# Optimization experiments

Measured on AMD Instinct MI355X. Metric: run time of the kernel, lower is better.

Reference implementation:

```python
import jax, jax.numpy as jnp
import numpy as np

D_MODEL = 512
HIDDEN = 2048
NUM_EXPERTS = 8
TOP_K = 2
BATCH, SEQ = 4, 4096


def setup_inputs() -> dict:
    key = jax.random.key(0)
    kx, kg, k1, k2 = jax.random.split(key, 4)
    x = jax.random.normal(kx, (BATCH, SEQ, D_MODEL), dtype=jnp.float32)
    # gate: nn.Linear(d_model, num_experts, bias=False), init std=0.02
    Wg = 0.02 * jax.random.normal(kg, (NUM_EXPERTS, D_MODEL), dtype=jnp.float32)
    # expert weights, xavier_uniform scale
    lim1 = float(np.sqrt(6.0 / (D_MODEL + HIDDEN)))
    lim2 = float(np.sqrt(6.0 / (HIDDEN + D_MODEL)))
    W1 = jax.random.uniform(k1, (NUM_EXPERTS, D_MODEL, HIDDEN), dtype=jnp.float32, minval=-lim1, maxval=lim1)
    W2 = jax.random.uniform(k2, (NUM_EXPERTS, HIDDEN, D_MODEL), dtype=jnp.float32, minval=-lim2, maxval=lim2)
    return {"x": x, "Wg": Wg, "W1": W1, "W2": W2}


def reference(x, Wg, W1, W2):
    B, S, d = x.shape
    E = W1.shape[0]
    xf = x.reshape(-1, d)  # [T, d]
    router_logits = xf @ Wg.T  # [T, E]
    # top-k routing, softmax over selected logits
    topv, sel = jax.lax.top_k(router_logits, TOP_K)  # [T, K]
    rw = jax.nn.softmax(topv, axis=-1)  # [T, K]
    # dense combine weights [T, E]: weight for expert e if selected, else 0
    cw = jnp.sum(jax.nn.one_hot(sel, E, dtype=xf.dtype) * rw[..., None], axis=1)
    # per-expert MLP (loop over small fixed E), weighted combine
    out = jnp.zeros_like(xf)
    for e in range(E):
        h = jax.nn.gelu(xf @ W1[e], approximate=False)  # exact erf GELU like nn.GELU
        out = out + cw[:, e:e + 1] * (h @ W2[e])
    return out.reshape(B, S, d), router_logits.reshape(B, S, E)
```

## Files before the change

kernel.cpp:

```cpp
#include <hip/hip_runtime.h>
#include <hip/hip_bf16.h>
#include <math.h>

#define T_TOK 16384
#define DM 512
#define HID 2048
#define NE 8
#define MT 64
#define CH 256
#define NCH (HID / CH)

typedef unsigned short u16;
typedef unsigned long long u64;
typedef __attribute__((ext_vector_type(4))) float f32x4;
typedef __attribute__((ext_vector_type(8))) __bf16 bf16x8;

static __device__ __forceinline__ u16 f2bf(float f) {
    __hip_bfloat16 h = __float2bfloat16(f);
    union { __hip_bfloat16 h; u16 u; } c; c.h = h; return c.u;
}

static __device__ __forceinline__ bf16x8 as_bf16x8(uint4 u) {
    union { uint4 u; bf16x8 b; } c; c.u = u; return c.b;
}

__global__ __launch_bounds__(256) void transpose_cvt(const float* __restrict__ in,
                                                     u16* __restrict__ out, int R, int C) {
    __shared__ float tile[64][65];
    const float* inp = in + (size_t)blockIdx.z * R * C;
    u16* outp = out + (size_t)blockIdx.z * R * C;
    int c0 = blockIdx.x * 64, r0 = blockIdx.y * 64;
    int tr = threadIdx.x >> 4;
    int tc = threadIdx.x & 15;
#pragma unroll
    for (int i = 0; i < 4; i++) {
        int r = i * 16 + tr;
        float4 v = *(const float4*)(inp + (size_t)(r0 + r) * C + c0 + tc * 4);
        tile[r][tc * 4 + 0] = v.x; tile[r][tc * 4 + 1] = v.y;
        tile[r][tc * 4 + 2] = v.z; tile[r][tc * 4 + 3] = v.w;
    }
    __syncthreads();
#pragma unroll
    for (int i = 0; i < 4; i++) {
        int c = i * 16 + tr;
        ushort4 o;
        o.x = f2bf(tile[tc * 4 + 0][c]); o.y = f2bf(tile[tc * 4 + 1][c]);
        o.z = f2bf(tile[tc * 4 + 2][c]); o.w = f2bf(tile[tc * 4 + 3][c]);
        *(ushort4*)(outp + (size_t)(c0 + c) * R + r0 + tc * 4) = o;
    }
}

__global__ __launch_bounds__(256) void router_kernel(
    const float* __restrict__ x, const float* __restrict__ Wg,
    float* __restrict__ logits, int* __restrict__ cnt,
    int* __restrict__ tlist, float* __restrict__ wlist, u16* __restrict__ xb)
{
    __shared__ int   s_sel[128];
    __shared__ float s_w[128];
    const int wave = threadIdx.x >> 6, lane = threadIdx.x & 63;
    const int tbase = blockIdx.x * 64;

    for (int i = 0; i < 16; i++) {
        int ti = wave * 16 + i;
        int t  = tbase + ti;
        const float4* xp = (const float4*)(x + (size_t)t * DM) + lane * 2;
        float4 a0 = xp[0], a1 = xp[1];
        union { u16 s[8]; uint4 v; } px;
        px.s[0] = f2bf(a0.x); px.s[1] = f2bf(a0.y); px.s[2] = f2bf(a0.z); px.s[3] = f2bf(a0.w);
        px.s[4] = f2bf(a1.x); px.s[5] = f2bf(a1.y); px.s[6] = f2bf(a1.z); px.s[7] = f2bf(a1.w);
        *(uint4*)(xb + (size_t)t * DM + lane * 8) = px.v;

        float acc[NE];
#pragma unroll
        for (int e = 0; e < NE; e++) {
            const float4* wp = (const float4*)(Wg + e * DM) + lane * 2;
            float4 b0 = wp[0], b1 = wp[1];
            acc[e] = a0.x*b0.x + a0.y*b0.y + a0.z*b0.z + a0.w*b0.w
                   + a1.x*b1.x + a1.y*b1.y + a1.z*b1.z + a1.w*b1.w;
        }
#pragma unroll
        for (int e = 0; e < NE; e++) {
#pragma unroll
            for (int off = 32; off >= 1; off >>= 1)
                acc[e] += __shfl_xor(acc[e], off, 64);
        }
        if (lane == 0) {
            float4* lg = (float4*)(logits + (size_t)t * NE);
            lg[0] = make_float4(acc[0], acc[1], acc[2], acc[3]);
            lg[1] = make_float4(acc[4], acc[5], acc[6], acc[7]);
            int i0 = 0; float v0 = acc[0];
#pragma unroll
            for (int e = 1; e < NE; e++) if (acc[e] > v0) { v0 = acc[e]; i0 = e; }
            int i1 = -1; float v1 = -1e30f;
#pragma unroll
            for (int e = 0; e < NE; e++) if (e != i0 && acc[e] > v1) { v1 = acc[e]; i1 = e; }
            float w0 = 1.f / (1.f + expf(v1 - v0));
            s_sel[ti * 2] = i0; s_sel[ti * 2 + 1] = i1;
            s_w[ti * 2] = w0;   s_w[ti * 2 + 1] = 1.f - w0;
        }
    }
    __syncthreads();
    if (wave == 0) {
        int s0 = s_sel[lane * 2], s1 = s_sel[lane * 2 + 1];
        float w0 = s_w[lane * 2], w1 = s_w[lane * 2 + 1];
        u64 A = 0, B = 0, C = 0;
        int myTot = 0;
#pragma unroll
        for (int e = 0; e < NE; e++) {
            u64 q0 = __ballot(s0 == e);
            u64 q1 = __ballot(s1 == e);
            if (s0 == e) A = q0;
            if (s1 == e) { B = q0; C = q1; }
            if (lane == e) myTot = __popcll(q0) + __popcll(q1);
        }
        int base = 0;
        if (lane < NE) base = atomicAdd(&cnt[lane], myTot);
        u64 below = ((u64)1 << lane) - 1;
        int b0 = __shfl(base, s0, 64);
        int b1 = __shfl(base, s1, 64);
        int t = tbase + lane;
        int slot0 = b0 + __popcll(A & below);
        int slot1 = b1 + __popcll(B) + __popcll(C & below);
        tlist[s0 * T_TOK + slot0] = t; wlist[s0 * T_TOK + slot0] = w0;
        tlist[s1 * T_TOK + slot1] = t; wlist[s1 * T_TOK + slot1] = w1;
    }
}

__global__ __launch_bounds__(512, 2) void expert_kernel(
    const u16* __restrict__ xb, const u16* __restrict__ W1T, const u16* __restrict__ W2T,
    const int* __restrict__ cnt, const int* __restrict__ tlist, const float* __restrict__ wlist,
    float* __restrict__ out)
{
    const int e = blockIdx.x & 7;
    const int tile = blockIdx.x >> 3;
    const int n = cnt[e];
    const int row0 = tile * MT;
    if (row0 >= n) return;
    const int wid = threadIdx.x >> 6;
    const int lane = threadIdx.x & 63;
    const int l15 = lane & 15, lhi = lane >> 4;
    const int* tl = tlist + e * T_TOK;

    __shared__ char xs[MT * 1024];
    __shared__ char hs[2][MT * CH * 2];

#pragma unroll
    for (int i = 0; i < 8; i++) {
        int r = wid * 8 + i;
        int idx = row0 + r;
        int tok = (idx < n) ? tl[idx] : 0;
        uint4 v = *(const uint4*)(xb + (size_t)tok * DM + lane * 8);
        *(uint4*)(xs + r * 1024 + ((lane * 16) ^ ((r & 7) << 4))) = v;
    }
    __syncthreads();

    f32x4 acc2[4][4];
#pragma unroll
    for (int m = 0; m < 4; m++)
#pragma unroll
        for (int nt = 0; nt < 4; nt++) acc2[m][nt] = (f32x4)0.0f;

    const u16* w1p = W1T + (size_t)e * HID * DM + (size_t)(wid * 32 + l15) * DM + lhi * 8;
    const u16* w2p = W2T + (size_t)e * DM * HID + (size_t)(wid * 64 + l15) * HID + lhi * 8;

    int xrow[4], hrow[4], swz[4];
#pragma unroll
    for (int m = 0; m < 4; m++) {
        int r = m * 16 + l15;
        xrow[m] = r * 1024;
        hrow[m] = r * (CH * 2);
        swz[m]  = (r & 7) << 4;
    }

    for (int ch = 0; ch < NCH; ++ch) {
        f32x4 acc1[2][4];
#pragma unroll
        for (int ht = 0; ht < 2; ht++)
#pragma unroll
            for (int m = 0; m < 4; m++) acc1[ht][m] = (f32x4)0.0f;
        const u16* bp1 = w1p + (size_t)ch * CH * DM;
#pragma unroll
        for (int ks = 0; ks < 16; ++ks) {
            bf16x8 w1a = as_bf16x8(*(const uint4*)(bp1 + ks * 32));
            bf16x8 w1b = as_bf16x8(*(const uint4*)(bp1 + 16 * DM + ks * 32));
            int colb = ks * 64 + lhi * 16;
#pragma unroll
            for (int m = 0; m < 4; ++m) {
                bf16x8 bx = *(const bf16x8*)(xs + xrow[m] + (colb ^ swz[m]));
                acc1[0][m] = __builtin_amdgcn_mfma_f32_16x16x32_bf16(w1a, bx, acc1[0][m], 0, 0, 0);
                acc1[1][m] = __builtin_amdgcn_mfma_f32_16x16x32_bf16(w1b, bx, acc1[1][m], 0, 0, 0);
            }
        }
        char* hw = hs[ch & 1];
#pragma unroll
        for (int ht = 0; ht < 2; ++ht) {
#pragma unroll
            for (int m = 0; m < 4; ++m) {
                union { ushort4 s; uint2 v; } p;
                float v0 = acc1[ht][m][0], v1 = acc1[ht][m][1];
                float v2 = acc1[ht][m][2], v3 = acc1[ht][m][3];
                p.s.x = f2bf(0.5f * v0 * (1.0f + erff(v0 * 0.70710678f)));
                p.s.y = f2bf(0.5f * v1 * (1.0f + erff(v1 * 0.70710678f)));
                p.s.z = f2bf(0.5f * v2 * (1.0f + erff(v2 * 0.70710678f)));
                p.s.w = f2bf(0.5f * v3 * (1.0f + erff(v3 * 0.70710678f)));
                *(uint2*)(hw + hrow[m] + ((wid * 64 + ht * 32 + lhi * 8) ^ swz[m])) = p.v;
            }
        }
        __syncthreads();
        const char* hr = hs[ch & 1];
        const u16* bp2 = w2p + ch * CH;
#pragma unroll
        for (int k2 = 0; k2 < 8; ++k2) {
            int colb = k2 * 64 + lhi * 16;
            bf16x8 a2[4];
#pragma unroll
            for (int m = 0; m < 4; ++m)
                a2[m] = *(const bf16x8*)(hr + hrow[m] + (colb ^ swz[m]));
#pragma unroll
            for (int nt = 0; nt < 4; ++nt) {
                bf16x8 b = as_bf16x8(*(const uint4*)(bp2 + (size_t)nt * 16 * HID + k2 * 32));
#pragma unroll
                for (int m = 0; m < 4; ++m)
                    acc2[m][nt] = __builtin_amdgcn_mfma_f32_16x16x32_bf16(a2[m], b, acc2[m][nt], 0, 0, 0);
            }
        }
    }

    const float* wl = wlist + e * T_TOK;
#pragma unroll
    for (int m = 0; m < 4; ++m) {
#pragma unroll
        for (int j = 0; j < 4; ++j) {
            int r = m * 16 + lhi * 4 + j;
            int idx = row0 + r;
            if (idx < n) {
                int tok = tl[idx];
                float w = wl[idx];
                float* op = out + (size_t)tok * DM + wid * 64 + l15;
#pragma unroll
                for (int nt = 0; nt < 4; ++nt)
                    atomicAdd(op + nt * 16, acc2[m][nt][j] * w);
            }
        }
    }
}

extern "C" void kernel_launch(void* const* d_in, const int* in_sizes, int n_in,
                              void* d_out, int out_size, void* d_ws, size_t ws_size,
                              hipStream_t stream) {
    const float* x  = (const float*)d_in[0];
    const float* Wg = (const float*)d_in[1];
    const float* W1 = (const float*)d_in[2];
    const float* W2 = (const float*)d_in[3];
    float* out = (float*)d_out;
    char* ws = (char*)d_ws;

    int*   cnt   = (int*)ws;
    int*   tlist = (int*)(ws + 1024);
    float* wlist = (float*)(ws + 1024 + NE * T_TOK * 4);
    u16*   xb    = (u16*)(ws + (2u << 20));
    u16*   W1T   = xb + (size_t)T_TOK * DM;
    u16*   W2T   = W1T + (size_t)NE * DM * HID;

    hipMemsetAsync(cnt, 0, 64, stream);
    hipMemsetAsync(out, 0, (size_t)T_TOK * DM * sizeof(float), stream);

    transpose_cvt<<<dim3(HID / 64, DM / 64, NE), 256, 0, stream>>>(W1, W1T, DM, HID);
    transpose_cvt<<<dim3(DM / 64, HID / 64, NE), 256, 0, stream>>>(W2, W2T, HID, DM);
    router_kernel<<<T_TOK / 64, 256, 0, stream>>>(x, Wg, out + (size_t)T_TOK * DM,
                                                  cnt, tlist, wlist, xb);
    expert_kernel<<<(T_TOK / MT) * NE, 512, 0, stream>>>(xb, W1T, W2T,
                                                         cnt, tlist, wlist, out);
}
```

Measured before the change: 647.8 us.

## Halve hidden chunk, single-buffer h tile, prefetch weights, raise occupancy

Cuts the hidden chunk size from 256 to 128 and switches the h tile in shared memory from double to single buffering, adding an extra barrier before the write. Each wave now computes one 16-column W1 slice instead of two, which shrinks accumulator registers, and the launch bound asks for 4 blocks per SM instead of 2. W1 and W2 fragments are now register-prefetched one k-step ahead to hide global load latency. In exchange there are twice as many chunk iterations and barriers, so each barrier amortizes less MFMA work. Register pressure could also force spills under the tighter bound.

```diff
diff --git a/kernel.cpp b/kernel.cpp
--- a/kernel.cpp
+++ b/kernel.cpp
@@ -7,7 +7,7 @@
 #define HID 2048
 #define NE 8
 #define MT 64
-#define CH 256
+#define CH 128
 #define NCH (HID / CH)
 
 typedef unsigned short u16;
@@ -126,7 +126,7 @@
     }
 }
 
-__global__ __launch_bounds__(512, 2) void expert_kernel(
+__global__ __launch_bounds__(512, 4) void expert_kernel(
     const u16* __restrict__ xb, const u16* __restrict__ W1T, const u16* __restrict__ W2T,
     const int* __restrict__ cnt, const int* __restrict__ tlist, const float* __restrict__ wlist,
     float* __restrict__ out)
@@ -142,7 +142,7 @@
     const int* tl = tlist + e * T_TOK;
 
     __shared__ char xs[MT * 1024];
-    __shared__ char hs[2][MT * CH * 2];
+    __shared__ char hs[MT * CH * 2];
 
 #pragma unroll
     for (int i = 0; i < 8; i++) {
@@ -152,7 +152,6 @@
         uint4 v = *(const uint4*)(xb + (size_t)tok * DM + lane * 8);
         *(uint4*)(xs + r * 1024 + ((lane * 16) ^ ((r & 7) << 4))) = v;
     }
-    __syncthreads();
 
     f32x4 acc2[4][4];
 #pragma unroll
@@ -160,7 +159,7 @@
 #pragma unroll
         for (int nt = 0; nt < 4; nt++) acc2[m][nt] = (f32x4)0.0f;
 
-    const u16* w1p = W1T + (size_t)e * HID * DM + (size_t)(wid * 32 + l15) * DM + lhi * 8;
+    const u16* w1p = W1T + (size_t)e * HID * DM + (size_t)(wid * 16 + l15) * DM + lhi * 8;
     const u16* w2p = W2T + (size_t)e * DM * HID + (size_t)(wid * 64 + l15) * HID + lhi * 8;
 
     int xrow[4], hrow[4], swz[4];
@@ -171,54 +170,66 @@
         hrow[m] = r * (CH * 2);
         swz[m]  = (r & 7) << 4;
     }
+    const int hwcol = wid * 32 + lhi * 8;
+
+    __syncthreads();
 
     for (int ch = 0; ch < NCH; ++ch) {
-        f32x4 acc1[2][4];
-#pragma unroll
-        for (int ht = 0; ht < 2; ht++)
-#pragma unroll
-            for (int m = 0; m < 4; m++) acc1[ht][m] = (f32x4)0.0f;
+        f32x4 acc1[4];
+#pragma unroll
+        for (int m = 0; m < 4; m++) acc1[m] = (f32x4)0.0f;
         const u16* bp1 = w1p + (size_t)ch * CH * DM;
+        uint4 w1n = *(const uint4*)(bp1);
 #pragma unroll
         for (int ks = 0; ks < 16; ++ks) {
-            bf16x8 w1a = as_bf16x8(*(const uint4*)(bp1 + ks * 32));
-            bf16x8 w1b = as_bf16x8(*(const uint4*)(bp1 + 16 * DM + ks * 32));
+            bf16x8 w1cur = as_bf16x8(w1n);
+            if (ks < 15) w1n = *(const uint4*)(bp1 + (ks + 1) * 32);
             int colb = ks * 64 + lhi * 16;
 #pragma unroll
             for (int m = 0; m < 4; ++m) {
                 bf16x8 bx = *(const bf16x8*)(xs + xrow[m] + (colb ^ swz[m]));
-                acc1[0][m] = __builtin_amdgcn_mfma_f32_16x16x32_bf16(w1a, bx, acc1[0][m], 0, 0, 0);
-                acc1[1][m] = __builtin_amdgcn_mfma_f32_16x16x32_bf16(w1b, bx, acc1[1][m], 0, 0, 0);
-            }
-        }
-        char* hw = hs[ch & 1];
-#pragma unroll
-        for (int ht = 0; ht < 2; ++ht) {
-#pragma unroll
-            for (int m = 0; m < 4; ++m) {
-                union { ushort4 s; uint2 v; } p;
-                float v0 = acc1[ht][m][0], v1 = acc1[ht][m][1];
-                float v2 = acc1[ht][m][2], v3 = acc1[ht][m][3];
-                p.s.x = f2bf(0.5f * v0 * (1.0f + erff(v0 * 0.70710678f)));
-                p.s.y = f2bf(0.5f * v1 * (1.0f + erff(v1 * 0.70710678f)));
-                p.s.z = f2bf(0.5f * v2 * (1.0f + erff(v2 * 0.70710678f)));
-                p.s.w = f2bf(0.5f * v3 * (1.0f + erff(v3 * 0.70710678f)));
-                *(uint2*)(hw + hrow[m] + ((wid * 64 + ht * 32 + lhi * 8) ^ swz[m])) = p.v;
-            }
+                acc1[m] = __builtin_amdgcn_mfma_f32_16x16x32_bf16(w1cur, bx, acc1[m], 0, 0, 0);
+            }
+        }
+        uint2 pk[4];
+#pragma unroll
+        for (int m = 0; m < 4; ++m) {
+            union { ushort4 s; uint2 v; } p;
+            float v0 = acc1[m][0], v1 = acc1[m][1], v2 = acc1[m][2], v3 = acc1[m][3];
+            p.s.x = f2bf(0.5f * v0 * (1.0f + erff(v0 * 0.70710678f)));
+            p.s.y = f2bf(0.5f * v1 * (1.0f + erff(v1 * 0.70710678f)));
+            p.s.z = f2bf(0.5f * v2 * (1.0f + erff(v2 * 0.70710678f)));
+            p.s.w = f2bf(0.5f * v3 * (1.0f + erff(v3 * 0.70710678f)));
+            pk[m] = p.v;
         }
         __syncthreads();
-        const char* hr = hs[ch & 1];
+#pragma unroll
+        for (int m = 0; m < 4; ++m)
+            *(uint2*)(hs + hrow[m] + (hwcol ^ swz[m])) = pk[m];
+        __syncthreads();
         const u16* bp2 = w2p + ch * CH;
-#pragma unroll
-        for (int k2 = 0; k2 < 8; ++k2) {
+        uint4 nb[4];
+#pragma unroll
+        for (int nt = 0; nt < 4; ++nt)
+            nb[nt] = *(const uint4*)(bp2 + (size_t)nt * 16 * HID);
+#pragma unroll
+        for (int k2 = 0; k2 < 4; ++k2) {
+            uint4 cur[4];
+#pragma unroll
+            for (int nt = 0; nt < 4; ++nt) cur[nt] = nb[nt];
+            if (k2 < 3) {
+#pragma unroll
+                for (int nt = 0; nt < 4; ++nt)
+                    nb[nt] = *(const uint4*)(bp2 + (size_t)nt * 16 * HID + (k2 + 1) * 32);
+            }
             int colb = k2 * 64 + lhi * 16;
             bf16x8 a2[4];
 #pragma unroll
             for (int m = 0; m < 4; ++m)
-                a2[m] = *(const bf16x8*)(hr + hrow[m] + (colb ^ swz[m]));
+                a2[m] = *(const bf16x8*)(hs + hrow[m] + (colb ^ swz[m]));
 #pragma unroll
             for (int nt = 0; nt < 4; ++nt) {
-                bf16x8 b = as_bf16x8(*(const uint4*)(bp2 + (size_t)nt * 16 * HID + k2 * 32));
+                bf16x8 b = as_bf16x8(cur[nt]);
 #pragma unroll
                 for (int m = 0; m < 4; ++m)
                     acc2[m][nt] = __builtin_amdgcn_mfma_f32_16x16x32_bf16(a2[m], b, acc2[m][nt], 0, 0, 0);
```

Result: slower. 916.1 us (+41.4%).
